# Optimization experiments

Measured on AMD Instinct MI355X. Metric: run time of the kernel, lower is better.

The kernel has to match this reference:

```python
import jax, jax.numpy as jnp
import numpy as np

NUM_POINTS = 32
NUM_RESIDUALS = 2
DIST_THRESHOLD = 5.0
H = W = 128
C = 16


def setup_inputs() -> dict:
    key = jax.random.key(0)
    k = jax.random.split(key, 6)
    return {
        "md_maps": jax.random.uniform(k[0], (1, 3, H, W), dtype=jnp.float32),
        "dis_maps": jax.random.uniform(k[1], (1, 1, H, W), dtype=jnp.float32),
        "residual_maps": jax.random.uniform(k[2], (1, 1, H, W), dtype=jnp.float32),
        "features": jax.random.normal(k[3], (C, H, W), dtype=jnp.float32),
        "jloc": jax.random.uniform(k[4], (1, H, W), dtype=jnp.float32),
        "joff": jax.random.uniform(k[5], (2, H, W), dtype=jnp.float32),
        "topk": 300,
    }


def hafm_decoding(md_maps, dis_maps, residual_maps):
    scale = DIST_THRESHOLD
    b, _, h, w = md_maps.shape
    y0, x0 = jnp.meshgrid(jnp.arange(h, dtype=jnp.float32),
                          jnp.arange(w, dtype=jnp.float32), indexing='ij')
    y0 = y0[None, None]
    x0 = x0[None, None]
    sign_pad = jnp.arange(-NUM_RESIDUALS, NUM_RESIDUALS + 1, dtype=jnp.float32).reshape(1, -1, 1, 1)
    dist = jnp.clip(dis_maps + residual_maps * sign_pad, 0.0, 1.0)  # [B, 2R+1, H, W]
    md_un = (md_maps[:, :1] - 0.5) * np.pi * 2.0
    st_un = md_maps[:, 1:2] * np.pi / 2.0
    ed_un = -md_maps[:, 2:3] * np.pi / 2.0
    cs_md = jnp.cos(md_un)
    ss_md = jnp.sin(md_un)
    y_st = jnp.tan(st_un)
    y_ed = jnp.tan(ed_un)
    x_st_final = jnp.clip((cs_md - ss_md * y_st) * dist * scale + x0, 0.0, w - 1)
    y_st_final = jnp.clip((ss_md + cs_md * y_st) * dist * scale + y0, 0.0, h - 1)
    x_ed_final = jnp.clip((cs_md - ss_md * y_ed) * dist * scale + x0, 0.0, w - 1)
    y_ed_final = jnp.clip((ss_md + cs_md * y_ed) * dist * scale + y0, 0.0, h - 1)
    lines = jnp.stack((x_st_final, y_st_final, x_ed_final, y_ed_final), axis=-1)
    return lines.reshape(b, -1, 4)  # [B, (2R+1)*H*W, 4]


def compute_loi_features(features_per_image, lines_per_im, tspan):
    c, h, w = features_per_image.shape
    U, V = lines_per_im[:, :2], lines_per_im[:, 2:]
    pts = U[:, :, None] * tspan + V[:, :, None] * (1.0 - tspan) - 0.5  # [N, 2, P]
    pts = pts.transpose(0, 2, 1).reshape(-1, 2)  # [N*P, 2]
    px, py = pts[:, 0], pts[:, 1]
    px0 = jnp.clip(jnp.floor(px), 0.0, w - 1)
    py0 = jnp.clip(jnp.floor(py), 0.0, h - 1)
    px1 = jnp.clip(px0 + 1.0, 0.0, w - 1)
    py1 = jnp.clip(py0 + 1.0, 0.0, h - 1)
    px0l, py0l = px0.astype(jnp.int32), py0.astype(jnp.int32)
    px1l, py1l = px1.astype(jnp.int32), py1.astype(jnp.int32)
    xp = (features_per_image[:, py0l, px0l] * (py1 - py) * (px1 - px)
          + features_per_image[:, py1l, px0l] * (py - py0) * (px1 - px)
          + features_per_image[:, py0l, px1l] * (py1 - py) * (px - px0)
          + features_per_image[:, py1l, px1l] * (py - py0) * (px - px0))  # [C, N*P]
    xp = xp.reshape(c, -1, tspan.size).transpose(1, 0, 2)  # [N, C, P]
    return xp.reshape(xp.shape[0], -1)  # [N, C*P]


def non_maximum_suppression(a):
    # a: [B, 1, H, W]; torch max_pool2d pads with -inf for max pooling
    ap = jax.lax.reduce_window(a, -jnp.inf, jax.lax.max, (1, 1, 3, 3), (1, 1, 1, 1),
                               [(0, 0), (0, 0), (1, 1), (1, 1)])
    return a * (a == ap).astype(a.dtype)


def get_junctions(jloc, joff, topk):
    h, w = jloc.shape[-2], jloc.shape[-1]
    flat = jloc.reshape(-1)
    joff2 = joff.reshape(2, -1)
    scores, index = jax.lax.top_k(flat, topk)
    y = (index // w).astype(jnp.float32) + joff2[1][index] + 0.5
    x = (index % w).astype(jnp.float32) + joff2[0][index] + 0.5
    junctions = jnp.stack((x, y), axis=1)  # [topk, 2]
    return junctions, scores


def reference(md_maps, dis_maps, residual_maps, features, jloc, joff, topk):
    tspan = jnp.linspace(0.0, 1.0, NUM_POINTS, dtype=jnp.float32)[None, None, :]
    lines = hafm_decoding(md_maps, dis_maps, residual_maps)  # [1, 5*H*W, 4]
    loi = compute_loi_features(features, lines[0], tspan)    # [5*H*W, C*P]
    jloc_nms = non_maximum_suppression(jloc[None])            # [1, 1, H, W]
    junctions, scores = get_junctions(jloc_nms[0], joff, topk)
    return loi, junctions, scores
```

## Files before the change

kernel.cpp:

```cpp
#include <hip/hip_runtime.h>
#include <math.h>

#define HPX 128
#define WPX 128
#define HW  16384
#define CCH 16
#define NLINES 81920
#define NPTS 32
#define LOI_SIZE (NLINES * 512)
#define SORT_N 8192
#define NBINS 4096
#define CAND 1024

#define FEAT_T_OFF 0
#define LINES_OFF  1048576
#define KEYS_OFF   (1048576 + 1310720)
#define HIST_OFF   (KEYS_OFF + 65536)
#define CTR_OFF    (HIST_OFF + 16384)

__global__ __launch_bounds__(256) void transpose_feat(
        const float* __restrict__ feat, float* __restrict__ feat_t) {
    int tid = blockIdx.x * 256 + threadIdx.x;
    int pix = tid >> 4;
    int c   = tid & 15;
    feat_t[tid] = feat[c * HW + pix];
}

__global__ __launch_bounds__(256) void lines_kernel(
        const float* __restrict__ md,
        const float* __restrict__ dis,
        const float* __restrict__ res,
        float4* __restrict__ lines) {
    int line = blockIdx.x * 256 + threadIdx.x;
    int r    = line >> 14;
    int pix  = line & (HW - 1);
    int y0i  = pix >> 7, x0i = pix & 127;

    float md0 = md[pix], md1 = md[HW + pix], md2 = md[2 * HW + pix];
    float dv  = dis[pix], rv = res[pix];

    float dist = fminf(fmaxf(dv + rv * ((float)r - 2.0f), 0.0f), 1.0f);
    float d5   = dist * 5.0f;
    float md_un = (md0 - 0.5f) * 6.28318530717958647692f;
    float cs = cosf(md_un), ss = sinf(md_un);
    float y_st = tanf(md1 * 1.57079632679489661923f);
    float y_ed = tanf(-md2 * 1.57079632679489661923f);

    float x0f = (float)x0i, y0f = (float)y0i;
    float4 ep;
    ep.x = fminf(fmaxf((cs - ss * y_st) * d5 + x0f, 0.0f), 127.0f);
    ep.y = fminf(fmaxf((ss + cs * y_st) * d5 + y0f, 0.0f), 127.0f);
    ep.z = fminf(fmaxf((cs - ss * y_ed) * d5 + x0f, 0.0f), 127.0f);
    ep.w = fminf(fmaxf((ss + cs * y_ed) * d5 + y0f, 0.0f), 127.0f);
    lines[line] = ep;
}

__global__ __launch_bounds__(256) void nms_compact(
        const float* __restrict__ jloc,
        unsigned long long* __restrict__ keys,
        unsigned int* __restrict__ hist,
        unsigned int* __restrict__ ctr) {
    int pix = blockIdx.x * 256 + threadIdx.x;
    if (pix >= HW) return;
    int y = pix >> 7, x = pix & 127;
    float a = jloc[pix];
    float m = a;
    #pragma unroll
    for (int dy = -1; dy <= 1; dy++) {
        #pragma unroll
        for (int dx = -1; dx <= 1; dx++) {
            int yy = y + dy, xx = x + dx;
            if (yy >= 0 && yy < HPX && xx >= 0 && xx < WPX) {
                m = fmaxf(m, jloc[yy * WPX + xx]);
            }
        }
    }
    if (a == m && a > 0.0f) {
        unsigned int slot = atomicAdd(ctr, 1u);
        if (slot < SORT_N) {
            unsigned int bits = __float_as_uint(a);
            keys[slot] = ((unsigned long long)bits << 32)
                       | (unsigned long long)(0xFFFFFFFFu - (unsigned int)pix);
        }
        int bin = min(NBINS - 1, (int)(a * (float)NBINS));
        atomicAdd(&hist[bin], 1u);
    }
}

__global__ __launch_bounds__(1024) void select_topk(
        const unsigned long long* __restrict__ keys_g,
        const unsigned int* __restrict__ ctr,
        const unsigned int* __restrict__ hist,
        const float* __restrict__ joff,
        float* __restrict__ junc, float* __restrict__ scores, int topk) {
    __shared__ unsigned int h[NBINS];
    __shared__ unsigned long long cand[CAND];
    __shared__ unsigned int scount;
    __shared__ int Ts;
    int t = threadIdx.x;

    #pragma unroll
    for (int r = 0; r < 4; r++) h[t + r * 1024] = hist[t + r * 1024];
    if (t == 0) { scount = 0; Ts = 0; }
    __syncthreads();

    for (int off = 1; off < NBINS; off <<= 1) {
        unsigned int v[4];
        #pragma unroll
        for (int r = 0; r < 4; r++) {
            int i = t + r * 1024;
            v[r] = (i + off < NBINS) ? h[i + off] : 0u;
        }
        __syncthreads();
        #pragma unroll
        for (int r = 0; r < 4; r++) h[t + r * 1024] += v[r];
        __syncthreads();
    }

    #pragma unroll
    for (int r = 0; r < 4; r++) {
        int b = t + r * 1024;
        unsigned int sb = h[b];
        unsigned int sn = (b + 1 < NBINS) ? h[b + 1] : 0u;
        if (sb >= (unsigned int)topk && sn < (unsigned int)topk) Ts = b;
    }
    __syncthreads();
    int T = Ts;

    int n = min(ctr[0], (unsigned int)SORT_N);
    for (int i = t; i < n; i += 1024) {
        unsigned long long kk = keys_g[i];
        float val = __uint_as_float((unsigned int)(kk >> 32));
        int bin = min(NBINS - 1, (int)(val * (float)NBINS));
        if (bin >= T) {
            unsigned int p = atomicAdd(&scount, 1u);
            if (p < CAND) cand[p] = kk;
        }
    }
    __syncthreads();
    unsigned int sc = min(scount, (unsigned int)CAND);
    if (t >= (int)sc) cand[t] = 0ull;
    __syncthreads();

    for (int k = 2; k <= CAND; k <<= 1) {
        for (int j = k >> 1; j > 0; j >>= 1) {
            int ixj = t ^ j;
            if (ixj > t) {
                unsigned long long a = cand[t], b = cand[ixj];
                bool desc = ((t & k) == 0);
                if (desc ? (a < b) : (a > b)) { cand[t] = b; cand[ixj] = a; }
            }
            __syncthreads();
        }
    }

    if (t < topk) {
        unsigned long long kk = cand[t];
        float val = __uint_as_float((unsigned int)(kk >> 32));
        unsigned int idx = 0xFFFFFFFFu - (unsigned int)(kk & 0xFFFFFFFFull);
        if (idx >= HW) idx = 0;
        float xo = joff[idx];
        float yo = joff[HW + idx];
        junc[2 * t]     = (float)(idx & 127) + xo + 0.5f;
        junc[2 * t + 1] = (float)(idx >> 7)  + yo + 0.5f;
        scores[t] = val;
    }
}

__global__ __launch_bounds__(256) void loi_kernel(
        const float4* __restrict__ lines,
        const float4* __restrict__ feat4,
        float* __restrict__ out) {
    int tid  = blockIdx.x * 256 + threadIdx.x;
    int cq   = tid & 3;
    int p    = (tid >> 2) & 31;
    int line = tid >> 7;

    float4 ep = lines[line];

    float tk = (float)p * (1.0f / 31.0f);
    float px = ep.x * tk + ep.z * (1.0f - tk) - 0.5f;
    float py = ep.y * tk + ep.w * (1.0f - tk) - 0.5f;

    float px0 = fminf(fmaxf(floorf(px), 0.0f), 127.0f);
    float py0 = fminf(fmaxf(floorf(py), 0.0f), 127.0f);
    float px1 = fminf(px0 + 1.0f, 127.0f);
    float py1 = fminf(py0 + 1.0f, 127.0f);

    float wx1 = px - px0, wx0 = px1 - px;
    float wy1 = py - py0, wy0 = py1 - py;
    float w00 = wy0 * wx0, w01 = wy0 * wx1;
    float w10 = wy1 * wx0, w11 = wy1 * wx1;

    int r0 = ((int)py0) * WPX;
    int r1 = ((int)py1) * WPX;
    int c0 = (int)px0;
    int c1 = (int)px1;

    float4 a = feat4[(r0 + c0) * 4 + cq];
    float4 b = feat4[(r0 + c1) * 4 + cq];
    float4 c = feat4[(r1 + c0) * 4 + cq];
    float4 d = feat4[(r1 + c1) * 4 + cq];

    float v0 = a.x * w00 + b.x * w01 + c.x * w10 + d.x * w11;
    float v1 = a.y * w00 + b.y * w01 + c.y * w10 + d.y * w11;
    float v2 = a.z * w00 + b.z * w01 + c.z * w10 + d.z * w11;
    float v3 = a.w * w00 + b.w * w01 + c.w * w10 + d.w * w11;

    float* ob = out + (size_t)line * 512 + cq * 128 + p;
    __builtin_nontemporal_store(v0, ob);
    __builtin_nontemporal_store(v1, ob + 32);
    __builtin_nontemporal_store(v2, ob + 64);
    __builtin_nontemporal_store(v3, ob + 96);
}

extern "C" void kernel_launch(void* const* d_in, const int* in_sizes, int n_in,
                              void* d_out, int out_size, void* d_ws, size_t ws_size,
                              hipStream_t stream) {
    const float* md   = (const float*)d_in[0];
    const float* dis  = (const float*)d_in[1];
    const float* res  = (const float*)d_in[2];
    const float* feat = (const float*)d_in[3];
    const float* jloc = (const float*)d_in[4];
    const float* joff = (const float*)d_in[5];
    int topk = (out_size - LOI_SIZE) / 3;

    char* ws = (char*)d_ws;
    float* feat_t             = (float*)(ws + FEAT_T_OFF);
    float4* lines             = (float4*)(ws + LINES_OFF);
    unsigned long long* keys  = (unsigned long long*)(ws + KEYS_OFF);
    unsigned int* hist        = (unsigned int*)(ws + HIST_OFF);
    unsigned int* ctr         = (unsigned int*)(ws + CTR_OFF);

    float* out    = (float*)d_out;
    float* junc   = out + LOI_SIZE;
    float* scores = junc + 2 * topk;

    hipMemsetAsync(ws + HIST_OFF, 0, NBINS * 4 + 4, stream);

    transpose_feat<<<(HW * CCH) / 256, 256, 0, stream>>>(feat, feat_t);
    lines_kernel <<<NLINES / 256,      256, 0, stream>>>(md, dis, res, lines);
    nms_compact  <<<HW / 256,          256, 0, stream>>>(jloc, keys, hist, ctr);
    select_topk  <<<1,                1024, 0, stream>>>(keys, ctr, hist, joff, junc, scores, topk);
    loi_kernel   <<<(NLINES * 128) / 256, 256, 0, stream>>>(
                     lines, (const float4*)feat_t, out);
}
```

Baseline: 230.8 us.

## Fuse transpose, line decoding and workspace reset; replace bitonic sort with rank selection

Merges the feature transpose and line-endpoint decoding into one launch, which also zeroes the histogram and counter, so the memset and one kernel launch go away. In select_topk, the 1024-wide bitonic sort with many barriers is replaced by a rank count: each candidate counts how many keys are larger and writes itself directly to that output slot. This trades O(n log^2 n) barrier-bound work for O(n) shared-memory reads per thread. Slots past the candidate count are filled with a default junction.

New measurement: 218.4 us. -5.4%, faster.

```diff
diff --git a/kernel.cpp b/kernel.cpp
--- a/kernel.cpp
+++ b/kernel.cpp
@@ -11,6 +11,7 @@
 #define SORT_N 8192
 #define NBINS 4096
 #define CAND 1024
+#define PREP_TRANS (HW * CCH)
 
 #define FEAT_T_OFF 0
 #define LINES_OFF  1048576
@@ -18,41 +19,47 @@
 #define HIST_OFF   (KEYS_OFF + 65536)
 #define CTR_OFF    (HIST_OFF + 16384)
 
-__global__ __launch_bounds__(256) void transpose_feat(
-        const float* __restrict__ feat, float* __restrict__ feat_t) {
-    int tid = blockIdx.x * 256 + threadIdx.x;
-    int pix = tid >> 4;
-    int c   = tid & 15;
-    feat_t[tid] = feat[c * HW + pix];
-}
-
-__global__ __launch_bounds__(256) void lines_kernel(
+__global__ __launch_bounds__(256) void prep_kernel(
+        const float* __restrict__ feat, float* __restrict__ feat_t,
         const float* __restrict__ md,
         const float* __restrict__ dis,
         const float* __restrict__ res,
-        float4* __restrict__ lines) {
-    int line = blockIdx.x * 256 + threadIdx.x;
-    int r    = line >> 14;
-    int pix  = line & (HW - 1);
-    int y0i  = pix >> 7, x0i = pix & 127;
-
-    float md0 = md[pix], md1 = md[HW + pix], md2 = md[2 * HW + pix];
-    float dv  = dis[pix], rv = res[pix];
-
-    float dist = fminf(fmaxf(dv + rv * ((float)r - 2.0f), 0.0f), 1.0f);
-    float d5   = dist * 5.0f;
-    float md_un = (md0 - 0.5f) * 6.28318530717958647692f;
-    float cs = cosf(md_un), ss = sinf(md_un);
-    float y_st = tanf(md1 * 1.57079632679489661923f);
-    float y_ed = tanf(-md2 * 1.57079632679489661923f);
-
-    float x0f = (float)x0i, y0f = (float)y0i;
-    float4 ep;
-    ep.x = fminf(fmaxf((cs - ss * y_st) * d5 + x0f, 0.0f), 127.0f);
-    ep.y = fminf(fmaxf((ss + cs * y_st) * d5 + y0f, 0.0f), 127.0f);
-    ep.z = fminf(fmaxf((cs - ss * y_ed) * d5 + x0f, 0.0f), 127.0f);
-    ep.w = fminf(fmaxf((ss + cs * y_ed) * d5 + y0f, 0.0f), 127.0f);
-    lines[line] = ep;
+        float4* __restrict__ lines,
+        unsigned int* __restrict__ hist,
+        unsigned int* __restrict__ ctr) {
+    int tid = blockIdx.x * 256 + threadIdx.x;
+
+    if (tid < NBINS) hist[tid] = 0u;
+    if (tid == NBINS) ctr[0] = 0u;
+
+    if (tid < PREP_TRANS) {
+        int pix = tid >> 4;
+        int c   = tid & 15;
+        feat_t[tid] = feat[c * HW + pix];
+    } else {
+        int line = tid - PREP_TRANS;
+        int r    = line >> 14;
+        int pix  = line & (HW - 1);
+        int y0i  = pix >> 7, x0i = pix & 127;
+
+        float md0 = md[pix], md1 = md[HW + pix], md2 = md[2 * HW + pix];
+        float dv  = dis[pix], rv = res[pix];
+
+        float dist = fminf(fmaxf(dv + rv * ((float)r - 2.0f), 0.0f), 1.0f);
+        float d5   = dist * 5.0f;
+        float md_un = (md0 - 0.5f) * 6.28318530717958647692f;
+        float cs = cosf(md_un), ss = sinf(md_un);
+        float y_st = tanf(md1 * 1.57079632679489661923f);
+        float y_ed = tanf(-md2 * 1.57079632679489661923f);
+
+        float x0f = (float)x0i, y0f = (float)y0i;
+        float4 ep;
+        ep.x = fminf(fmaxf((cs - ss * y_st) * d5 + x0f, 0.0f), 127.0f);
+        ep.y = fminf(fmaxf((ss + cs * y_st) * d5 + y0f, 0.0f), 127.0f);
+        ep.z = fminf(fmaxf((cs - ss * y_ed) * d5 + x0f, 0.0f), 127.0f);
+        ep.w = fminf(fmaxf((ss + cs * y_ed) * d5 + y0f, 0.0f), 127.0f);
+        lines[line] = ep;
+    }
 }
 
 __global__ __launch_bounds__(256) void nms_compact(
@@ -139,31 +146,26 @@
     }
     __syncthreads();
     unsigned int sc = min(scount, (unsigned int)CAND);
-    if (t >= (int)sc) cand[t] = 0ull;
-    __syncthreads();
-
-    for (int k = 2; k <= CAND; k <<= 1) {
-        for (int j = k >> 1; j > 0; j >>= 1) {
-            int ixj = t ^ j;
-            if (ixj > t) {
-                unsigned long long a = cand[t], b = cand[ixj];
-                bool desc = ((t & k) == 0);
-                if (desc ? (a < b) : (a > b)) { cand[t] = b; cand[ixj] = a; }
-            }
-            __syncthreads();
-        }
-    }
-
-    if (t < topk) {
-        unsigned long long kk = cand[t];
-        float val = __uint_as_float((unsigned int)(kk >> 32));
-        unsigned int idx = 0xFFFFFFFFu - (unsigned int)(kk & 0xFFFFFFFFull);
-        if (idx >= HW) idx = 0;
-        float xo = joff[idx];
-        float yo = joff[HW + idx];
-        junc[2 * t]     = (float)(idx & 127) + xo + 0.5f;
-        junc[2 * t + 1] = (float)(idx >> 7)  + yo + 0.5f;
-        scores[t] = val;
+
+    if (t < (int)sc) {
+        unsigned long long k = cand[t];
+        int r = 0;
+        for (unsigned int j = 0; j < sc; j++) r += (cand[j] > k) ? 1 : 0;
+        if (r < topk) {
+            float val = __uint_as_float((unsigned int)(k >> 32));
+            unsigned int idx = 0xFFFFFFFFu - (unsigned int)(k & 0xFFFFFFFFull);
+            if (idx >= HW) idx = 0;
+            float xo = joff[idx];
+            float yo = joff[HW + idx];
+            junc[2 * r]     = (float)(idx & 127) + xo + 0.5f;
+            junc[2 * r + 1] = (float)(idx >> 7)  + yo + 0.5f;
+            scores[r] = val;
+        }
+    }
+    if (t >= (int)sc && t < topk) {
+        junc[2 * t]     = joff[0] + 0.5f;
+        junc[2 * t + 1] = joff[HW] + 0.5f;
+        scores[t] = 0.0f;
     }
 }
 
@@ -236,12 +238,10 @@
     float* junc   = out + LOI_SIZE;
     float* scores = junc + 2 * topk;
 
-    hipMemsetAsync(ws + HIST_OFF, 0, NBINS * 4 + 4, stream);
-
-    transpose_feat<<<(HW * CCH) / 256, 256, 0, stream>>>(feat, feat_t);
-    lines_kernel <<<NLINES / 256,      256, 0, stream>>>(md, dis, res, lines);
-    nms_compact  <<<HW / 256,          256, 0, stream>>>(jloc, keys, hist, ctr);
-    select_topk  <<<1,                1024, 0, stream>>>(keys, ctr, hist, joff, junc, scores, topk);
-    loi_kernel   <<<(NLINES * 128) / 256, 256, 0, stream>>>(
-                     lines, (const float4*)feat_t, out);
-}
+    prep_kernel <<<(PREP_TRANS + NLINES) / 256, 256, 0, stream>>>(
+                    feat, feat_t, md, dis, res, lines, hist, ctr);
+    nms_compact <<<HW / 256, 256, 0, stream>>>(jloc, keys, hist, ctr);
+    select_topk <<<1, 1024, 0, stream>>>(keys, ctr, hist, joff, junc, scores, topk);
+    loi_kernel  <<<(NLINES * 128) / 256, 256, 0, stream>>>(
+                    lines, (const float4*)feat_t, out);
+}
```
